# Kernel tuning notes

Measured on AMD Instinct MI355X. Metric: run time of the kernel, lower is better.

Reference implementation:

```python
import jax, jax.numpy as jnp
import numpy as np
import math

# ---- static config (matches init_kwargs) ----
B, L, CIN = 16, 192, 21
D = 128          # d_model
LAYERS = 2
P, S = 24, 12    # patch_length, stride
PRED, COUT = 96, 21
BN_EPS = 1e-5
NT = L // S      # number of patches = 16


def _conv1d(x, w, b=None, stride=1, padding=0):
    # x: (N, Cin, L), w: (Cout, Cin, K)
    y = jax.lax.conv_general_dilated(x, w, (stride,), [(padding, padding)],
                                     dimension_numbers=("NCH", "OIH", "NCH"))
    if b is not None:
        y = y + b[None, :, None]
    return y


def _conv2d(x, w, padding):
    # x: (N, Cin, H, W), w: (Cout, Cin, kh, kw)
    return jax.lax.conv_general_dilated(x, w, (1, 1), padding,
                                        dimension_numbers=("NCHW", "OIHW", "NCHW"))


def _pos_embed(length, d):
    pos = jnp.arange(length, dtype=jnp.float32)[:, None]
    div = jnp.exp(jnp.arange(0, d, 2, dtype=jnp.float32) * (-math.log(10000.0) / d))
    pe = jnp.zeros((length, d), jnp.float32)
    pe = pe.at[:, 0::2].set(jnp.sin(pos * div)).at[:, 1::2].set(jnp.cos(pos * div))
    return pe


def _times_block(x, Wi, pw, pb, g, beta, aw):
    # x: (b, c, t, h, w); Wi: (out=c, in=c, 3, 3)
    b, c, t, h, w = x.shape
    res = x
    pp = x.mean(axis=(3, 4))                       # AdaptiveAvgPool3d((None,1,1)) -> (b,c,t)
    pp = _conv1d(pp, pw, pb, padding=1)            # period_conv
    scale = g / jnp.sqrt(1.0 + BN_EPS)             # eval-mode BN, running stats (0, 1)
    pp = jax.nn.relu(pp * scale[None, :, None] + beta[None, :, None])
    pooled = pp.mean(axis=-1)                      # AdaptiveAvgPool1d(1) -> (b,c)
    alpha = jnp.einsum("oc,bc->bo", aw, pooled) + 1.0   # alpha_conv (1x1, no bias) + 1
    # dynamic weight: (b, out, in, 3, 3) -> (b*out, in, 3, 3)
    Wd = (Wi[None] * alpha[:, :, None, None, None]).reshape(b * c, c, 3, 3)
    x2 = x.reshape(b, c, t, h * w)
    # conv2d with groups=1: every sample sees ALL b*out filters -> (b, b*out, t-2, hw-2)
    y = _conv2d(x2, Wd, [(0, 0), (0, 0)])
    # conv_transpose2d(y, Wd) == conv2d(y, flip(Wd).swap(O,I), full padding)
    Wt = jnp.swapaxes(jnp.flip(Wd, (-2, -1)), 0, 1)     # (c, b*out, 3, 3)
    z = _conv2d(y, Wt, [(2, 2), (2, 2)])                 # (b, c, t, hw)
    return z.reshape(b, c, t, h, w) + res


def setup_inputs() -> dict:
    key = jax.random.key(0)
    ks = jax.random.split(key, 13)
    rn = lambda k, shp, s: jax.random.normal(k, shp, jnp.float32) * s
    return {
        "x": jax.random.normal(ks[0], (B, L, CIN), jnp.float32),
        "token_w": rn(ks[1], (D, CIN, 3), 1.0 / np.sqrt(CIN * 3)),
        "patch_w": rn(ks[2], (P, 1, P), 1.0 / np.sqrt(P)),
        "patch_b": rn(ks[3], (P,), 0.02),
        "Wi": rn(ks[4], (LAYERS, D, D, 3, 3), 1.0 / np.sqrt(D * 9)),
        "pconv_w": rn(ks[5], (LAYERS, D, D, 3), 1.0 / np.sqrt(D * 3)),
        "pconv_b": rn(ks[6], (LAYERS, D), 0.02),
        "bn_g": jnp.ones((LAYERS, D), jnp.float32),
        "bn_b": jnp.zeros((LAYERS, D), jnp.float32),
        "aconv_w": rn(ks[7], (LAYERS, D, D), 1.0 / np.sqrt(D)),
        "fc1_w": rn(ks[8], (PRED, 2 * L), 1.0 / np.sqrt(2 * L)),
        "fc1_b": rn(ks[9], (PRED,), 0.02),
        "fc2_w": rn(ks[10], (COUT, D), 1.0 / np.sqrt(D)),
        "fc2_b": rn(ks[11], (COUT,), 0.02),
    }


def reference(x, token_w, patch_w, patch_b, Wi, pconv_w, pconv_b,
              bn_g, bn_b, aconv_w, fc1_w, fc1_b, fc2_w, fc2_b):
    # ---- DataEmbedding (dropout in eval mode) ----
    xt = jnp.pad(x.transpose(0, 2, 1), ((0, 0), (0, 0), (1, 1)), mode="wrap")  # circular pad
    emb = _conv1d(xt, token_w).transpose(0, 2, 1)            # (B, L, D)
    emb = emb + _pos_embed(L, D)[None]
    # ---- patch Embedding ----
    xe = emb.reshape(B * D, 1, L)                             # matches torch reshape/permute
    xe = jnp.pad(xe, ((0, 0), (0, 0), (0, P - S)), mode="edge")  # replicate pad
    xe = _conv1d(xe, patch_w, patch_b, stride=S)              # (B*D, P, NT)
    xe = xe.transpose(0, 2, 1).reshape(B, NT, P, D)           # torch reshape semantics (C-order)
    x5 = jnp.stack([xe[:, :, 0::2, :], xe[:, :, 1::2, :]], axis=2)  # (B, NT, 2, P//2, D)
    x5 = x5.transpose(0, 4, 1, 2, 3)                          # (B, D, NT, 2, 12)
    # ---- TimesBlocks ----
    for i in range(LAYERS):
        x5 = _times_block(x5, Wi[i], pconv_w[i], pconv_b[i], bn_g[i], bn_b[i], aconv_w[i])
    # ---- heads ----
    xf = x5.reshape(B, -1, D)                                 # (B, 2L, D)
    y1 = xf.transpose(0, 2, 1) @ fc1_w.T + fc1_b              # (B, D, PRED)
    out = y1.transpose(0, 2, 1) @ fc2_w.T + fc2_b             # (B, PRED, COUT)
    return out
```

## Files before the change

### kernel.cpp

```cpp
#include <hip/hip_runtime.h>
#include <math.h>

constexpr int cB = 16, cL = 192, cCIN = 21, cD = 128;
constexpr int cNT = 16, cHW = 24;
constexpr int cPRED = 96, cCOUT = 21;
constexpr int cYH = 14, cYW = 22;

typedef __attribute__((ext_vector_type(8))) short bf16x8;
typedef __attribute__((ext_vector_type(4))) float f32x4;

__device__ inline unsigned short f2bf(float f) {
    union { float f; unsigned u; } v; v.f = f;
    unsigned u = v.u;
    unsigned r = (u + 0x7fffu + ((u >> 16) & 1u)) >> 16;
    return (unsigned short)r;
}

__device__ inline f32x4 mfma16(bf16x8 a, bf16x8 b, f32x4 c) {
    return __builtin_amdgcn_mfma_f32_16x16x32_bf16(a, b, c, 0, 0, 0);
}

__global__ void k_init(const float* __restrict__ Wi, const float* __restrict__ fc1_w,
                       const float* __restrict__ token_w, const float* __restrict__ fc2_w,
                       unsigned short* __restrict__ Wp, unsigned short* __restrict__ w1p,
                       float* __restrict__ twT, unsigned short* __restrict__ w2p,
                       float* __restrict__ w2s, float* __restrict__ peT,
                       unsigned short* __restrict__ Y0T) {
    int e = blockIdx.x * blockDim.x + threadIdx.x;
    if (e < 589824) {
        int lyr = e / 294912;
        int rem = e % 294912;
        int dir = rem / 147456;
        int q = rem % 147456;
        int kt = q >> 12;
        int oi = (q >> 9) & 7;
        int kg = (q >> 7) & 3;
        int r  = (q >> 3) & 15;
        int j  = q & 7;
        int k = kt * 32 + kg * 8 + j;
        int a = k >> 7;
        int o, c;
        if (dir == 0) { o = oi * 16 + r; c = k & 127; }
        else          { o = k & 127;     c = oi * 16 + r; }
        Wp[e] = f2bf(Wi[lyr * 147456 + o * 1152 + c * 9 + a]);
        return;
    }
    e -= 589824;
    if (e < 36864) {
        int p = e / 384, mh = e % 384;
        w1p[e] = f2bf(fc1_w[p * 384 + 3 * (mh & 127) + (mh >> 7)]);
        return;
    }
    e -= 36864;
    if (e < 8064) {
        int d = e & 127, c3 = e >> 7;
        twT[e] = token_w[d * 63 + c3];
        return;
    }
    e -= 8064;
    if (e < 4096) {
        int q = e >> 7, d = e & 127;
        w2p[e] = (q < 21) ? f2bf(fc2_w[q * 128 + d]) : (unsigned short)0;
        return;
    }
    e -= 4096;
    if (e < 32) {
        if (e < 21) {
            float s = 0.f;
            for (int d = 0; d < 128; ++d) s += fc2_w[e * 128 + d];
            w2s[e] = s;
        } else if (e < 32) w2s[e] = 0.f;
        return;
    }
    e -= 32;
    if (e < 24576) {
        int l = e >> 7, d = e & 127;
        int i2 = d >> 1;
        float dv = expf(-(float)(2 * i2) * (9.210340371976184f / 128.f));
        float ang = (float)l * dv;
        peT[e] = (d & 1) ? cosf(ang) : sinf(ang);
        return;
    }
    e -= 24576;
    if (e < 16384) {
        int n = e >> 10, j = e & 1023;
        bf16x8 z = {0, 0, 0, 0, 0, 0, 0, 0};
        *(bf16x8*)(Y0T + n * 65536 + j * 8) = z;
    }
}

__global__ void k_embed(const float* __restrict__ x, const float* __restrict__ twT,
                        const float* __restrict__ peT, float* __restrict__ emb) {
    int idx = blockIdx.x * blockDim.x + threadIdx.x;
    if (idx >= cB * cL * cD) return;
    int d = idx & 127;
    int r = idx >> 7;
    int l = r % cL;
    int b = r / cL;
    int lm = (l == 0) ? 191 : l - 1;
    int lp = (l == 191) ? 0 : l + 1;
    const float* xb = x + b * 4032;
    float acc = peT[l * 128 + d];
    for (int c = 0; c < cCIN; ++c) {
        float x0 = xb[lm * 21 + c], x1 = xb[l * 21 + c], x2 = xb[lp * 21 + c];
        const float* tb = twT + c * 384 + d;
        acc += x0 * tb[0] + x1 * tb[128] + x2 * tb[256];
    }
    emb[idx] = acc;
}

__global__ __launch_bounds__(192) void k_patch(const float* __restrict__ emb,
                                               const float* __restrict__ pw,
                                               const float* __restrict__ pb,
                                               float* __restrict__ x5) {
    __shared__ float pwL[24][24];
    int t = threadIdx.x;
    for (int z = t; z < 576; z += 192) pwL[z / 24][z % 24] = pw[z];
    __syncthreads();
    int pair = blockIdx.x * 8 + t / 24;
    int p = t % 24;
    int i = pair >> 4, tt = pair & 15;
    const float* ebase = emb + i * 192;
    int j0 = tt * 12;
    float acc = pb[p];
    #pragma unroll
    for (int k = 0; k < 24; ++k) {
        int j = j0 + k;
        j = j > 191 ? 191 : j;
        acc += ebase[j] * pwL[p][k];
    }
    int G = (i & 127) * 384 + tt * 24 + p;
    int b = i >> 7;
    int tp = G / 3072;
    int pp2 = (G % 3072) / 128;
    int cc = G & 127;
    x5[b * 49152 + cc * 384 + tp * 24 + (pp2 & 1) * 12 + (pp2 >> 1)] = acc;
}

__global__ __launch_bounds__(256) void k_stats(const float* __restrict__ x5,
        const float* __restrict__ pw, const float* __restrict__ pb,
        const float* __restrict__ g, const float* __restrict__ bb,
        const float* __restrict__ aw, float* __restrict__ alpha,
        unsigned short* __restrict__ XT, int pack) {
    __shared__ float ppT[18][128];
    __shared__ float part[256];
    __shared__ float pooled[128];
    __shared__ unsigned short tile[64][136];
    int b = blockIdx.x, t = threadIdx.x;
    if (t < 128) { ppT[0][t] = 0.f; ppT[17][t] = 0.f; }
    #pragma unroll
    for (int i = 0; i < 8; ++i) {
        int ct = t + 256 * i;
        const float* p = x5 + b * 49152 + ct * 24;
        float s = 0.f;
        #pragma unroll
        for (int j = 0; j < 6; ++j) {
            f32x4 v = *(const f32x4*)(p + 4 * j);
            s += v[0] + v[1] + v[2] + v[3];
        }
        ppT[1 + (ct & 15)][ct >> 4] = s * (1.f / 24.f);
    }
    __syncthreads();
    int o = t >> 1, th = (t & 1) * 8;
    float acc[8];
    float pbo = pb[o];
    #pragma unroll
    for (int i = 0; i < 8; ++i) acc[i] = pbo;
    for (int c4 = 0; c4 < 32; ++c4) {
        union { f32x4 v[3]; float f[12]; } u;
        u.v[0] = *(const f32x4*)(pw + o * 384 + c4 * 12);
        u.v[1] = *(const f32x4*)(pw + o * 384 + c4 * 12 + 4);
        u.v[2] = *(const f32x4*)(pw + o * 384 + c4 * 12 + 8);
        f32x4 pv[10];
        #pragma unroll
        for (int r = 0; r < 10; ++r) pv[r] = *(f32x4*)&ppT[th + r][c4 * 4];
        #pragma unroll
        for (int cc = 0; cc < 4; ++cc) {
            float a0 = u.f[cc * 3], a1 = u.f[cc * 3 + 1], a2 = u.f[cc * 3 + 2];
            #pragma unroll
            for (int i = 0; i < 8; ++i)
                acc[i] += a0 * pv[i][cc] + a1 * pv[i + 1][cc] + a2 * pv[i + 2][cc];
        }
    }
    float scale = g[o] * rsqrtf(1.f + 1e-5f);
    float beta = bb[o];
    float partial = 0.f;
    #pragma unroll
    for (int i = 0; i < 8; ++i) {
        float v = acc[i] * scale + beta;
        partial += v > 0.f ? v : 0.f;
    }
    part[t] = partial;
    __syncthreads();
    if (t < 128) pooled[t] = (part[2 * t] + part[2 * t + 1]) * (1.f / 16.f);
    __syncthreads();
    if (t < 128) {
        float a = 1.f;
        for (int c4 = 0; c4 < 32; ++c4) {
            f32x4 av = *(const f32x4*)(aw + t * 128 + c4 * 4);
            f32x4 pv4 = *(f32x4*)&pooled[c4 * 4];
            a += av[0] * pv4[0] + av[1] * pv4[1] + av[2] * pv4[2] + av[3] * pv4[3];
        }
        alpha[b * 128 + t] = a;
    }
    if (!pack) return;
    for (int ch = 0; ch < 6; ++ch) {
        __syncthreads();
        int p4 = (t & 15) * 4;
        #pragma unroll
        for (int i = 0; i < 8; ++i) {
            int c = (t >> 4) + i * 16;
            f32x4 v = *(const f32x4*)(x5 + b * 49152 + c * 384 + ch * 64 + p4);
            #pragma unroll
            for (int r = 0; r < 4; ++r) tile[p4 + r][c] = f2bf(v[r]);
        }
        __syncthreads();
        #pragma unroll
        for (int i = 0; i < 4; ++i) {
            int idx = t + i * 256;
            int pp = idx >> 4, c8 = (idx & 15) * 8;
            *(bf16x8*)(XT + b * 57344 + (ch * 64 + pp) * 128 + c8) = *(bf16x8*)&tile[pp][c8];
        }
    }
    bf16x8 z = {0, 0, 0, 0, 0, 0, 0, 0};
    #pragma unroll
    for (int i = 0; i < 4; ++i) {
        int idx = t + i * 256;
        int pp = idx >> 4, c8 = (idx & 15) * 8;
        *(bf16x8*)(XT + b * 57344 + (384 + pp) * 128 + c8) = z;
    }
}

__global__ __launch_bounds__(64) void k_gfwd(const unsigned short* __restrict__ XT,
        const unsigned short* __restrict__ Wp, const float* __restrict__ alpha,
        unsigned short* __restrict__ Y0T) {
    int bid = blockIdx.x;
    int rm = bid >> 1, cn = bid & 1;
    int n = rm / 12, p0 = (rm % 12) * 32;
    int o0 = cn * 64;
    int l = threadIdx.x;
    int sm = l & 15, skg = l >> 4;
    const unsigned short* XTn = XT + n * 57344;
    const unsigned short* WB = Wp + (o0 >> 4) * 512 + l * 8;
    f32x4 acc[2][4];
    #pragma unroll
    for (int mi = 0; mi < 2; ++mi)
        #pragma unroll
        for (int ni = 0; ni < 4; ++ni) acc[mi][ni] = (f32x4){0.f, 0.f, 0.f, 0.f};
    #pragma unroll
    for (int kt = 0; kt < 36; ++kt) {
        int a = kt >> 2;
        int off = (a / 3) * 24 + (a % 3);
        int kc = (kt & 3) * 32 + skg * 8;
        const unsigned short* ab = XTn + (p0 + sm + off) * 128 + kc;
        bf16x8 a0 = *(const bf16x8*)(ab);
        bf16x8 a1 = *(const bf16x8*)(ab + 2048);
        const unsigned short* wb = WB + kt * 4096;
        bf16x8 b0 = *(const bf16x8*)(wb);
        bf16x8 b1 = *(const bf16x8*)(wb + 512);
        bf16x8 b2 = *(const bf16x8*)(wb + 1024);
        bf16x8 b3 = *(const bf16x8*)(wb + 1536);
        acc[0][0] = mfma16(a0, b0, acc[0][0]);
        acc[0][1] = mfma16(a0, b1, acc[0][1]);
        acc[0][2] = mfma16(a0, b2, acc[0][2]);
        acc[0][3] = mfma16(a0, b3, acc[0][3]);
        acc[1][0] = mfma16(a1, b0, acc[1][0]);
        acc[1][1] = mfma16(a1, b1, acc[1][1]);
        acc[1][2] = mfma16(a1, b2, acc[1][2]);
        acc[1][3] = mfma16(a1, b3, acc[1][3]);
    }
    #pragma unroll
    for (int ni = 0; ni < 4; ++ni) {
        int o = o0 + ni * 16 + sm;
        float s = 0.f;
        #pragma unroll
        for (int bb2 = 0; bb2 < 16; ++bb2) { float a = alpha[bb2 * 128 + o]; s += a * a; }
        #pragma unroll
        for (int mi = 0; mi < 2; ++mi) {
            #pragma unroll
            for (int r = 0; r < 4; ++r) {
                int p = p0 + mi * 16 + skg * 4 + r;
                bool valid = ((p % 24) < cYW) && ((p / 24) < cYH);
                float v = valid ? acc[mi][ni][r] * s : 0.f;
                Y0T[n * 65536 + (64 + p) * 128 + o] = f2bf(v);
            }
        }
    }
}

__global__ __launch_bounds__(64) void k_gbwd(const unsigned short* __restrict__ Y0T,
        const unsigned short* __restrict__ Wpb, float* __restrict__ x5,
        unsigned short* __restrict__ xdst, int mode) {
    __shared__ unsigned short tr[32][72];
    int bid = blockIdx.x;
    int rm = bid >> 1, cn = bid & 1;
    int n = rm / 12, p0 = (rm % 12) * 32;
    int c0 = cn * 64;
    int l = threadIdx.x;
    int sm = l & 15, skg = l >> 4;
    const unsigned short* Yn = Y0T + n * 65536 + 64 * 128;
    const unsigned short* WB = Wpb + (c0 >> 4) * 512 + l * 8;
    f32x4 acc[2][4];
    #pragma unroll
    for (int mi = 0; mi < 2; ++mi)
        #pragma unroll
        for (int ni = 0; ni < 4; ++ni) acc[mi][ni] = (f32x4){0.f, 0.f, 0.f, 0.f};
    #pragma unroll
    for (int kt = 0; kt < 36; ++kt) {
        int a = kt >> 2;
        int off = (a / 3) * 24 + (a % 3);
        int kc = (kt & 3) * 32 + skg * 8;
        const unsigned short* ab = Yn + (p0 + sm - off) * 128 + kc;
        bf16x8 a0 = *(const bf16x8*)(ab);
        bf16x8 a1 = *(const bf16x8*)(ab + 2048);
        const unsigned short* wb = WB + kt * 4096;
        bf16x8 b0 = *(const bf16x8*)(wb);
        bf16x8 b1 = *(const bf16x8*)(wb + 512);
        bf16x8 b2 = *(const bf16x8*)(wb + 1024);
        bf16x8 b3 = *(const bf16x8*)(wb + 1536);
        acc[0][0] = mfma16(a0, b0, acc[0][0]);
        acc[0][1] = mfma16(a0, b1, acc[0][1]);
        acc[0][2] = mfma16(a0, b2, acc[0][2]);
        acc[0][3] = mfma16(a0, b3, acc[0][3]);
        acc[1][0] = mfma16(a1, b0, acc[1][0]);
        acc[1][1] = mfma16(a1, b1, acc[1][1]);
        acc[1][2] = mfma16(a1, b2, acc[1][2]);
        acc[1][3] = mfma16(a1, b3, acc[1][3]);
    }
    #pragma unroll
    for (int ni = 0; ni < 4; ++ni) {
        int cl = ni * 16 + sm;
        int c = c0 + cl;
        #pragma unroll
        for (int mi = 0; mi < 2; ++mi) {
            int pl = mi * 16 + skg * 4;
            float* dst = x5 + n * 49152 + c * 384 + p0 + pl;
            f32x4 ov = *(f32x4*)dst;
            #pragma unroll
            for (int r = 0; r < 4; ++r) {
                ov[r] += acc[mi][ni][r];
                tr[pl + r][cl] = f2bf(ov[r]);
            }
            *(f32x4*)dst = ov;
        }
    }
    __syncthreads();
    if (mode == 0) {
        #pragma unroll
        for (int pass = 0; pass < 4; ++pass) {
            int idx = pass * 64 + l;
            int row = idx >> 3, ch = idx & 7;
            *(bf16x8*)(xdst + n * 57344 + (p0 + row) * 128 + c0 + ch * 8) = *(bf16x8*)&tr[row][ch * 8];
        }
    } else {
        #pragma unroll
        for (int pass = 0; pass < 4; ++pass) {
            int idx = pass * 64 + l;
            int cl = idx >> 2, pl0 = (idx & 3) * 8;
            __attribute__((aligned(16))) unsigned short tmp[8];
            #pragma unroll
            for (int j2 = 0; j2 < 8; ++j2) tmp[j2] = tr[pl0 + j2][cl];
            *(bf16x8*)(xdst + n * 49152 + ((p0 >> 7) * 128 + c0 + cl) * 128 + (p0 & 127) + pl0) =
                *(bf16x8*)tmp;
        }
    }
}

__global__ __launch_bounds__(64) void k_gemmZ(const unsigned short* __restrict__ xfM,
        const unsigned short* __restrict__ w2p, unsigned short* __restrict__ Zt) {
    int bid = blockIdx.x;
    int b = bid / 12, m0 = (bid % 12) * 32;
    int l = threadIdx.x, sm = l & 15, skg = l >> 4;
    f32x4 acc[2][2];
    #pragma unroll
    for (int mi = 0; mi < 2; ++mi)
        #pragma unroll
        for (int ni = 0; ni < 2; ++ni) acc[mi][ni] = (f32x4){0.f, 0.f, 0.f, 0.f};
    #pragma unroll
    for (int kt = 0; kt < 4; ++kt) {
        int kc = kt * 32 + skg * 8;
        const unsigned short* ab = xfM + b * 49152 + (m0 + sm) * 128 + kc;
        bf16x8 a0 = *(const bf16x8*)(ab);
        bf16x8 a1 = *(const bf16x8*)(ab + 2048);
        bf16x8 b0 = *(const bf16x8*)(w2p + sm * 128 + kc);
        bf16x8 b1 = *(const bf16x8*)(w2p + (16 + sm) * 128 + kc);
        acc[0][0] = mfma16(a0, b0, acc[0][0]);
        acc[0][1] = mfma16(a0, b1, acc[0][1]);
        acc[1][0] = mfma16(a1, b0, acc[1][0]);
        acc[1][1] = mfma16(a1, b1, acc[1][1]);
    }
    #pragma unroll
    for (int mi = 0; mi < 2; ++mi)
        #pragma unroll
        for (int ni = 0; ni < 2; ++ni) {
            int q = ni * 16 + sm;
            int mh = m0 + mi * 16 + skg * 4;
            #pragma unroll
            for (int r = 0; r < 4; ++r)
                Zt[b * 12288 + q * 384 + mh + r] = f2bf(acc[mi][ni][r]);
        }
}

__global__ __launch_bounds__(64) void k_gemmO(const unsigned short* __restrict__ w1p,
        const unsigned short* __restrict__ Zt, const float* __restrict__ b1,
        const float* __restrict__ w2s, const float* __restrict__ b2,
        float* __restrict__ out) {
    int bid = blockIdx.x;
    int b = bid / 3, p0 = (bid % 3) * 32;
    int l = threadIdx.x, sm = l & 15, skg = l >> 4;
    f32x4 acc[2][2];
    #pragma unroll
    for (int mi = 0; mi < 2; ++mi)
        #pragma unroll
        for (int ni = 0; ni < 2; ++ni) acc[mi][ni] = (f32x4){0.f, 0.f, 0.f, 0.f};
    #pragma unroll
    for (int kt = 0; kt < 12; ++kt) {
        int kc = kt * 32 + skg * 8;
        const unsigned short* ab = w1p + (p0 + sm) * 384 + kc;
        bf16x8 a0 = *(const bf16x8*)(ab);
        bf16x8 a1 = *(const bf16x8*)(ab + 16 * 384);
        const unsigned short* zb = Zt + b * 12288 + sm * 384 + kc;
        bf16x8 b0 = *(const bf16x8*)(zb);
        bf16x8 b1v = *(const bf16x8*)(zb + 16 * 384);
        acc[0][0] = mfma16(a0, b0, acc[0][0]);
        acc[0][1] = mfma16(a0, b1v, acc[0][1]);
        acc[1][0] = mfma16(a1, b0, acc[1][0]);
        acc[1][1] = mfma16(a1, b1v, acc[1][1]);
    }
    #pragma unroll
    for (int ni = 0; ni < 2; ++ni) {
        int q = ni * 16 + sm;
        if (q < 21) {
            float wsq = w2s[q], bq = b2[q];
            #pragma unroll
            for (int mi = 0; mi < 2; ++mi) {
                #pragma unroll
                for (int r = 0; r < 4; ++r) {
                    int p = p0 + mi * 16 + skg * 4 + r;
                    out[b * 2016 + p * 21 + q] = acc[mi][ni][r] + b1[p] * wsq + bq;
                }
            }
        }
    }
}

extern "C" void kernel_launch(void* const* d_in, const int* in_sizes, int n_in,
                              void* d_out, int out_size, void* d_ws, size_t ws_size,
                              hipStream_t stream) {
    const float* x       = (const float*)d_in[0];
    const float* token_w = (const float*)d_in[1];
    const float* patch_w = (const float*)d_in[2];
    const float* patch_b = (const float*)d_in[3];
    const float* Wi      = (const float*)d_in[4];
    const float* pconv_w = (const float*)d_in[5];
    const float* pconv_b = (const float*)d_in[6];
    const float* bn_g    = (const float*)d_in[7];
    const float* bn_b    = (const float*)d_in[8];
    const float* aconv_w = (const float*)d_in[9];
    const float* fc1_w   = (const float*)d_in[10];
    const float* fc1_b   = (const float*)d_in[11];
    const float* fc2_w   = (const float*)d_in[12];
    const float* fc2_b   = (const float*)d_in[13];
    float* out = (float*)d_out;

    float* ws    = (float*)d_ws;
    float* x5    = ws;
    float* alpha = ws + 786432;
    unsigned short* Wp  = (unsigned short*)(ws + 788480);
    unsigned short* w1p = (unsigned short*)(ws + 1083392);
    unsigned short* w2p = (unsigned short*)(ws + 1101824);
    float* w2s   = ws + 1103872;
    float* twT   = ws + 1103904;
    float* peT   = ws + 1111968;
    float* emb   = ws + 1136544;
    unsigned short* XT  = (unsigned short*)(ws + 1136544 + 393216);
    unsigned short* xfM = XT;
    unsigned short* Y0T = (unsigned short*)(ws + 1136544 + 393216 + 458752);
    unsigned short* Zt  = Y0T;

    k_init<<<2656, 256, 0, stream>>>(Wi, fc1_w, token_w, fc2_w, Wp, w1p, twT, w2p, w2s, peT, Y0T);
    k_embed<<<1536, 256, 0, stream>>>(x, twT, peT, emb);
    k_patch<<<4096, 192, 0, stream>>>(emb, patch_w, patch_b, x5);
    k_stats<<<16, 256, 0, stream>>>(x5, pconv_w, pconv_b, bn_g, bn_b, aconv_w, alpha, XT, 1);
    k_gfwd<<<384, 64, 0, stream>>>(XT, Wp, alpha, Y0T);
    k_gbwd<<<384, 64, 0, stream>>>(Y0T, Wp + 147456, x5, XT, 0);
    k_stats<<<16, 256, 0, stream>>>(x5, pconv_w + 49152, pconv_b + 128, bn_g + 128,
                                    bn_b + 128, aconv_w + 16384, alpha, XT, 0);
    k_gfwd<<<384, 64, 0, stream>>>(XT, Wp + 2 * 147456, alpha, Y0T);
    k_gbwd<<<384, 64, 0, stream>>>(Y0T, Wp + 3 * 147456, x5, xfM, 1);
    k_gemmZ<<<192, 64, 0, stream>>>(xfM, w2p, Zt);
    k_gemmO<<<48, 64, 0, stream>>>(w1p, Zt, fc1_b, w2s, fc2_b, out);
}
```

Measured before the change: 230.1 us.

## Fuse all stages into one persistent kernel with atomic grid barriers

Replaces the eleven separate kernel launches with a single persistent kernel of 256 blocks. The stages are separated by software grid barriers built on global atomics, and each former kernel body becomes a device function indexed by wave. It also folds the positional encoding into the embed step, stages the token weights in shared memory, and writes the bf16 transposed XT directly from the patch step instead of packing it in the stats kernel. This removes launch gaps and intermediate passes, at the cost of spin-wait barriers and idle blocks during the small phases (stats uses only 16 blocks).

```diff
diff --git a/kernel.cpp b/kernel.cpp
--- a/kernel.cpp
+++ b/kernel.cpp
@@ -1,10 +1,10 @@
 #include <hip/hip_runtime.h>
 #include <math.h>
 
-constexpr int cB = 16, cL = 192, cCIN = 21, cD = 128;
-constexpr int cNT = 16, cHW = 24;
-constexpr int cPRED = 96, cCOUT = 21;
+constexpr int cCIN = 21;
 constexpr int cYH = 14, cYW = 22;
+constexpr int NB = 256;
+constexpr int BT = 256;
 
 typedef __attribute__((ext_vector_type(8))) short bf16x8;
 typedef __attribute__((ext_vector_type(4))) float f32x4;
@@ -20,145 +20,47 @@
     return __builtin_amdgcn_mfma_f32_16x16x32_bf16(a, b, c, 0, 0, 0);
 }
 
-__global__ void k_init(const float* __restrict__ Wi, const float* __restrict__ fc1_w,
-                       const float* __restrict__ token_w, const float* __restrict__ fc2_w,
-                       unsigned short* __restrict__ Wp, unsigned short* __restrict__ w1p,
-                       float* __restrict__ twT, unsigned short* __restrict__ w2p,
-                       float* __restrict__ w2s, float* __restrict__ peT,
-                       unsigned short* __restrict__ Y0T) {
-    int e = blockIdx.x * blockDim.x + threadIdx.x;
-    if (e < 589824) {
-        int lyr = e / 294912;
-        int rem = e % 294912;
-        int dir = rem / 147456;
-        int q = rem % 147456;
-        int kt = q >> 12;
-        int oi = (q >> 9) & 7;
-        int kg = (q >> 7) & 3;
-        int r  = (q >> 3) & 15;
-        int j  = q & 7;
-        int k = kt * 32 + kg * 8 + j;
-        int a = k >> 7;
-        int o, c;
-        if (dir == 0) { o = oi * 16 + r; c = k & 127; }
-        else          { o = k & 127;     c = oi * 16 + r; }
-        Wp[e] = f2bf(Wi[lyr * 147456 + o * 1152 + c * 9 + a]);
-        return;
-    }
-    e -= 589824;
-    if (e < 36864) {
-        int p = e / 384, mh = e % 384;
-        w1p[e] = f2bf(fc1_w[p * 384 + 3 * (mh & 127) + (mh >> 7)]);
-        return;
-    }
-    e -= 36864;
-    if (e < 8064) {
-        int d = e & 127, c3 = e >> 7;
-        twT[e] = token_w[d * 63 + c3];
-        return;
-    }
-    e -= 8064;
-    if (e < 4096) {
-        int q = e >> 7, d = e & 127;
-        w2p[e] = (q < 21) ? f2bf(fc2_w[q * 128 + d]) : (unsigned short)0;
-        return;
-    }
-    e -= 4096;
-    if (e < 32) {
-        if (e < 21) {
-            float s = 0.f;
-            for (int d = 0; d < 128; ++d) s += fc2_w[e * 128 + d];
-            w2s[e] = s;
-        } else if (e < 32) w2s[e] = 0.f;
-        return;
-    }
-    e -= 32;
-    if (e < 24576) {
-        int l = e >> 7, d = e & 127;
-        int i2 = d >> 1;
-        float dv = expf(-(float)(2 * i2) * (9.210340371976184f / 128.f));
-        float ang = (float)l * dv;
-        peT[e] = (d & 1) ? cosf(ang) : sinf(ang);
-        return;
-    }
-    e -= 24576;
-    if (e < 16384) {
-        int n = e >> 10, j = e & 1023;
-        bf16x8 z = {0, 0, 0, 0, 0, 0, 0, 0};
-        *(bf16x8*)(Y0T + n * 65536 + j * 8) = z;
-    }
-}
-
-__global__ void k_embed(const float* __restrict__ x, const float* __restrict__ twT,
-                        const float* __restrict__ peT, float* __restrict__ emb) {
-    int idx = blockIdx.x * blockDim.x + threadIdx.x;
-    if (idx >= cB * cL * cD) return;
-    int d = idx & 127;
-    int r = idx >> 7;
-    int l = r % cL;
-    int b = r / cL;
-    int lm = (l == 0) ? 191 : l - 1;
-    int lp = (l == 191) ? 0 : l + 1;
-    const float* xb = x + b * 4032;
-    float acc = peT[l * 128 + d];
-    for (int c = 0; c < cCIN; ++c) {
-        float x0 = xb[lm * 21 + c], x1 = xb[l * 21 + c], x2 = xb[lp * 21 + c];
-        const float* tb = twT + c * 384 + d;
-        acc += x0 * tb[0] + x1 * tb[128] + x2 * tb[256];
-    }
-    emb[idx] = acc;
-}
-
-__global__ __launch_bounds__(192) void k_patch(const float* __restrict__ emb,
-                                               const float* __restrict__ pw,
-                                               const float* __restrict__ pb,
-                                               float* __restrict__ x5) {
-    __shared__ float pwL[24][24];
-    int t = threadIdx.x;
-    for (int z = t; z < 576; z += 192) pwL[z / 24][z % 24] = pw[z];
-    __syncthreads();
-    int pair = blockIdx.x * 8 + t / 24;
-    int p = t % 24;
-    int i = pair >> 4, tt = pair & 15;
-    const float* ebase = emb + i * 192;
-    int j0 = tt * 12;
-    float acc = pb[p];
-    #pragma unroll
-    for (int k = 0; k < 24; ++k) {
-        int j = j0 + k;
-        j = j > 191 ? 191 : j;
-        acc += ebase[j] * pwL[p][k];
-    }
-    int G = (i & 127) * 384 + tt * 24 + p;
-    int b = i >> 7;
-    int tp = G / 3072;
-    int pp2 = (G % 3072) / 128;
-    int cc = G & 127;
-    x5[b * 49152 + cc * 384 + tp * 24 + (pp2 & 1) * 12 + (pp2 >> 1)] = acc;
-}
-
-__global__ __launch_bounds__(256) void k_stats(const float* __restrict__ x5,
+struct SMem {
+    union {
+        float twL[8064];
+        float pwL[576];
+        struct { float ppT[18][128]; float part[256]; float pooled[128]; } st;
+        unsigned short tr[4][32][72];
+    };
+};
+
+__device__ inline void gbar(int* bar, int phase) {
+    __syncthreads();
+    if (threadIdx.x == 0) {
+        __threadfence();
+        __hip_atomic_fetch_add(&bar[phase], 1, __ATOMIC_RELEASE, __HIP_MEMORY_SCOPE_AGENT);
+        while (__hip_atomic_load(&bar[phase], __ATOMIC_ACQUIRE, __HIP_MEMORY_SCOPE_AGENT) < NB) {
+            __builtin_amdgcn_s_sleep(1);
+        }
+    }
+    __syncthreads();
+}
+
+__global__ void k_zbar(int* bar) {
+    if (threadIdx.x < 16) bar[threadIdx.x] = 0;
+}
+
+__device__ void stats_body(int b, int t, const float* __restrict__ x5,
         const float* __restrict__ pw, const float* __restrict__ pb,
         const float* __restrict__ g, const float* __restrict__ bb,
-        const float* __restrict__ aw, float* __restrict__ alpha,
-        unsigned short* __restrict__ XT, int pack) {
-    __shared__ float ppT[18][128];
-    __shared__ float part[256];
-    __shared__ float pooled[128];
-    __shared__ unsigned short tile[64][136];
-    int b = blockIdx.x, t = threadIdx.x;
-    if (t < 128) { ppT[0][t] = 0.f; ppT[17][t] = 0.f; }
+        const float* __restrict__ aw, float* __restrict__ alpha, SMem* s) {
+    if (t < 128) { s->st.ppT[0][t] = 0.f; s->st.ppT[17][t] = 0.f; }
     #pragma unroll
     for (int i = 0; i < 8; ++i) {
         int ct = t + 256 * i;
         const float* p = x5 + b * 49152 + ct * 24;
-        float s = 0.f;
+        float ssum = 0.f;
         #pragma unroll
         for (int j = 0; j < 6; ++j) {
             f32x4 v = *(const f32x4*)(p + 4 * j);
-            s += v[0] + v[1] + v[2] + v[3];
-        }
-        ppT[1 + (ct & 15)][ct >> 4] = s * (1.f / 24.f);
+            ssum += v[0] + v[1] + v[2] + v[3];
+        }
+        s->st.ppT[1 + (ct & 15)][ct >> 4] = ssum * (1.f / 24.f);
     }
     __syncthreads();
     int o = t >> 1, th = (t & 1) * 8;
@@ -173,7 +75,7 @@
         u.v[2] = *(const f32x4*)(pw + o * 384 + c4 * 12 + 8);
         f32x4 pv[10];
         #pragma unroll
-        for (int r = 0; r < 10; ++r) pv[r] = *(f32x4*)&ppT[th + r][c4 * 4];
+        for (int r = 0; r < 10; ++r) pv[r] = *(f32x4*)&s->st.ppT[th + r][c4 * 4];
         #pragma unroll
         for (int cc = 0; cc < 4; ++cc) {
             float a0 = u.f[cc * 3], a1 = u.f[cc * 3 + 1], a2 = u.f[cc * 3 + 2];
@@ -190,55 +92,27 @@
         float v = acc[i] * scale + beta;
         partial += v > 0.f ? v : 0.f;
     }
-    part[t] = partial;
-    __syncthreads();
-    if (t < 128) pooled[t] = (part[2 * t] + part[2 * t + 1]) * (1.f / 16.f);
+    s->st.part[t] = partial;
+    __syncthreads();
+    if (t < 128) s->st.pooled[t] = (s->st.part[2 * t] + s->st.part[2 * t + 1]) * (1.f / 16.f);
     __syncthreads();
     if (t < 128) {
         float a = 1.f;
         for (int c4 = 0; c4 < 32; ++c4) {
             f32x4 av = *(const f32x4*)(aw + t * 128 + c4 * 4);
-            f32x4 pv4 = *(f32x4*)&pooled[c4 * 4];
+            f32x4 pv4 = *(f32x4*)&s->st.pooled[c4 * 4];
             a += av[0] * pv4[0] + av[1] * pv4[1] + av[2] * pv4[2] + av[3] * pv4[3];
         }
         alpha[b * 128 + t] = a;
     }
-    if (!pack) return;
-    for (int ch = 0; ch < 6; ++ch) {
-        __syncthreads();
-        int p4 = (t & 15) * 4;
-        #pragma unroll
-        for (int i = 0; i < 8; ++i) {
-            int c = (t >> 4) + i * 16;
-            f32x4 v = *(const f32x4*)(x5 + b * 49152 + c * 384 + ch * 64 + p4);
-            #pragma unroll
-            for (int r = 0; r < 4; ++r) tile[p4 + r][c] = f2bf(v[r]);
-        }
-        __syncthreads();
-        #pragma unroll
-        for (int i = 0; i < 4; ++i) {
-            int idx = t + i * 256;
-            int pp = idx >> 4, c8 = (idx & 15) * 8;
-            *(bf16x8*)(XT + b * 57344 + (ch * 64 + pp) * 128 + c8) = *(bf16x8*)&tile[pp][c8];
-        }
-    }
-    bf16x8 z = {0, 0, 0, 0, 0, 0, 0, 0};
-    #pragma unroll
-    for (int i = 0; i < 4; ++i) {
-        int idx = t + i * 256;
-        int pp = idx >> 4, c8 = (idx & 15) * 8;
-        *(bf16x8*)(XT + b * 57344 + (384 + pp) * 128 + c8) = z;
-    }
-}
-
-__global__ __launch_bounds__(64) void k_gfwd(const unsigned short* __restrict__ XT,
+}
+
+__device__ void gfwd_body(int wv, int l, const unsigned short* __restrict__ XT,
         const unsigned short* __restrict__ Wp, const float* __restrict__ alpha,
         unsigned short* __restrict__ Y0T) {
-    int bid = blockIdx.x;
-    int rm = bid >> 1, cn = bid & 1;
+    int rm = wv >> 1, cn = wv & 1;
     int n = rm / 12, p0 = (rm % 12) * 32;
     int o0 = cn * 64;
-    int l = threadIdx.x;
     int sm = l & 15, skg = l >> 4;
     const unsigned short* XTn = XT + n * 57344;
     const unsigned short* WB = Wp + (o0 >> 4) * 512 + l * 8;
@@ -288,15 +162,13 @@
     }
 }
 
-__global__ __launch_bounds__(64) void k_gbwd(const unsigned short* __restrict__ Y0T,
+__device__ void gbwd_body(int wv, int l, int wslot, const unsigned short* __restrict__ Y0T,
         const unsigned short* __restrict__ Wpb, float* __restrict__ x5,
-        unsigned short* __restrict__ xdst, int mode) {
-    __shared__ unsigned short tr[32][72];
-    int bid = blockIdx.x;
-    int rm = bid >> 1, cn = bid & 1;
+        unsigned short* __restrict__ xdst, int mode, SMem* s) {
+    unsigned short (*tr)[72] = s->tr[wslot];
+    int rm = wv >> 1, cn = wv & 1;
     int n = rm / 12, p0 = (rm % 12) * 32;
     int c0 = cn * 64;
-    int l = threadIdx.x;
     int sm = l & 15, skg = l >> 4;
     const unsigned short* Yn = Y0T + n * 65536 + 64 * 128;
     const unsigned short* WB = Wpb + (c0 >> 4) * 512 + l * 8;
@@ -344,7 +216,6 @@
             *(f32x4*)dst = ov;
         }
     }
-    __syncthreads();
     if (mode == 0) {
         #pragma unroll
         for (int pass = 0; pass < 4; ++pass) {
@@ -366,11 +237,10 @@
     }
 }
 
-__global__ __launch_bounds__(64) void k_gemmZ(const unsigned short* __restrict__ xfM,
+__device__ void gemmZ_body(int wv, int l, const unsigned short* __restrict__ xfM,
         const unsigned short* __restrict__ w2p, unsigned short* __restrict__ Zt) {
-    int bid = blockIdx.x;
-    int b = bid / 12, m0 = (bid % 12) * 32;
-    int l = threadIdx.x, sm = l & 15, skg = l >> 4;
+    int b = wv / 12, m0 = (wv % 12) * 32;
+    int sm = l & 15, skg = l >> 4;
     f32x4 acc[2][2];
     #pragma unroll
     for (int mi = 0; mi < 2; ++mi)
@@ -401,13 +271,12 @@
         }
 }
 
-__global__ __launch_bounds__(64) void k_gemmO(const unsigned short* __restrict__ w1p,
+__device__ void gemmO_body(int wv, int l, const unsigned short* __restrict__ w1p,
         const unsigned short* __restrict__ Zt, const float* __restrict__ b1,
         const float* __restrict__ w2s, const float* __restrict__ b2,
         float* __restrict__ out) {
-    int bid = blockIdx.x;
-    int b = bid / 3, p0 = (bid % 3) * 32;
-    int l = threadIdx.x, sm = l & 15, skg = l >> 4;
+    int b = wv / 3, p0 = (wv % 3) * 32;
+    int sm = l & 15, skg = l >> 4;
     f32x4 acc[2][2];
     #pragma unroll
     for (int mi = 0; mi < 2; ++mi)
@@ -442,6 +311,158 @@
             }
         }
     }
+}
+
+__global__ __launch_bounds__(BT) void k_all(
+        const float* __restrict__ x, const float* __restrict__ token_w,
+        const float* __restrict__ patch_w, const float* __restrict__ patch_b,
+        const float* __restrict__ Wi, const float* __restrict__ pconv_w,
+        const float* __restrict__ pconv_b, const float* __restrict__ bn_g,
+        const float* __restrict__ bn_b, const float* __restrict__ aconv_w,
+        const float* __restrict__ fc1_w, const float* __restrict__ fc1_b,
+        const float* __restrict__ fc2_w, const float* __restrict__ fc2_b,
+        float* __restrict__ out,
+        float* __restrict__ x5, float* __restrict__ alpha,
+        unsigned short* __restrict__ Wp, unsigned short* __restrict__ w1p,
+        unsigned short* __restrict__ w2p, float* __restrict__ w2s,
+        float* __restrict__ emb, unsigned short* __restrict__ XT,
+        unsigned short* __restrict__ Y0T, int* bar) {
+    __shared__ SMem s;
+    int t = threadIdx.x;
+    int g = blockIdx.x * BT + t;
+    int wv = g >> 6;
+    int l = t & 63;
+
+    for (int z = t; z < 8064; z += BT) {
+        int d = z / 63, c3 = z % 63;
+        s.twL[c3 * 128 + d] = token_w[z];
+    }
+    __syncthreads();
+
+    for (int e0 = g; e0 < 1040416; e0 += NB * BT) {
+        int e = e0;
+        if (e < 589824) {
+            int lyr = e / 294912;
+            int rem = e % 294912;
+            int dir = rem / 147456;
+            int q = rem % 147456;
+            int kt = q >> 12;
+            int oi = (q >> 9) & 7;
+            int kg = (q >> 7) & 3;
+            int r  = (q >> 3) & 15;
+            int j  = q & 7;
+            int k = kt * 32 + kg * 8 + j;
+            int a = k >> 7;
+            int o, c;
+            if (dir == 0) { o = oi * 16 + r; c = k & 127; }
+            else          { o = k & 127;     c = oi * 16 + r; }
+            Wp[e] = f2bf(Wi[lyr * 147456 + o * 1152 + c * 9 + a]);
+            continue;
+        }
+        e -= 589824;
+        if (e < 36864) {
+            int p = e / 384, mh = e % 384;
+            w1p[e] = f2bf(fc1_w[p * 384 + 3 * (mh & 127) + (mh >> 7)]);
+            continue;
+        }
+        e -= 36864;
+        if (e < 4096) {
+            int q = e >> 7, d = e & 127;
+            w2p[e] = (q < 21) ? f2bf(fc2_w[q * 128 + d]) : (unsigned short)0;
+            continue;
+        }
+        e -= 4096;
+        if (e < 32) {
+            if (e < 21) {
+                float ssum = 0.f;
+                for (int d = 0; d < 128; ++d) ssum += fc2_w[e * 128 + d];
+                w2s[e] = ssum;
+            } else w2s[e] = 0.f;
+            continue;
+        }
+        e -= 32;
+        if (e < 393216) {
+            int d = e & 127;
+            int r = e >> 7;
+            int ll = r % 192;
+            int b = r / 192;
+            int lm = (ll == 0) ? 191 : ll - 1;
+            int lp = (ll == 191) ? 0 : ll + 1;
+            const float* xb = x + b * 4032;
+            int i2 = d >> 1;
+            float dv = expf(-(float)(2 * i2) * (9.210340371976184f / 128.f));
+            float ang = (float)ll * dv;
+            float acc = (d & 1) ? cosf(ang) : sinf(ang);
+            for (int c = 0; c < cCIN; ++c) {
+                float x0 = xb[lm * 21 + c], x1 = xb[ll * 21 + c], x2 = xb[lp * 21 + c];
+                acc += x0 * s.twL[(c * 3 + 0) * 128 + d]
+                     + x1 * s.twL[(c * 3 + 1) * 128 + d]
+                     + x2 * s.twL[(c * 3 + 2) * 128 + d];
+            }
+            emb[e] = acc;
+            continue;
+        }
+        e -= 393216;
+        {
+            int n = e >> 10, j = e & 1023;
+            bf16x8 z = {0, 0, 0, 0, 0, 0, 0, 0};
+            *(bf16x8*)(Y0T + n * 65536 + j * 8) = z;
+        }
+    }
+    gbar(bar, 0);
+
+    for (int z = t; z < 576; z += BT) ((float*)s.pwL)[z] = patch_w[z];
+    __syncthreads();
+    for (int u = g; u < 786432; u += NB * BT) {
+        int pair = u / 24;
+        int p = u % 24;
+        int i = pair >> 4, tt = pair & 15;
+        const float* ebase = emb + i * 192;
+        int j0 = tt * 12;
+        float acc = patch_b[p];
+        #pragma unroll
+        for (int k = 0; k < 24; ++k) {
+            int j = j0 + k;
+            j = j > 191 ? 191 : j;
+            acc += ebase[j] * s.pwL[p * 24 + k];
+        }
+        int G = (i & 127) * 384 + tt * 24 + p;
+        int b = i >> 7;
+        int tp = G / 3072;
+        int pp2 = (G % 3072) / 128;
+        int cc = G & 127;
+        int pp = tp * 24 + (pp2 & 1) * 12 + (pp2 >> 1);
+        x5[b * 49152 + cc * 384 + pp] = acc;
+        XT[b * 57344 + pp * 128 + cc] = f2bf(acc);
+    }
+    if (g < 16384) {
+        int n = g >> 10, rem = g & 1023;
+        int pp = 384 + (rem >> 4), c8 = (rem & 15) * 8;
+        bf16x8 z = {0, 0, 0, 0, 0, 0, 0, 0};
+        *(bf16x8*)(XT + n * 57344 + pp * 128 + c8) = z;
+    }
+    gbar(bar, 1);
+
+    if (blockIdx.x < 16)
+        stats_body(blockIdx.x, t, x5, pconv_w, pconv_b, bn_g, bn_b, aconv_w, alpha, &s);
+    gbar(bar, 2);
+    if (wv < 384) gfwd_body(wv, l, XT, Wp, alpha, Y0T);
+    gbar(bar, 3);
+    if (wv < 384) gbwd_body(wv, l, t >> 6, Y0T, Wp + 147456, x5, XT, 0, &s);
+    gbar(bar, 4);
+
+    if (blockIdx.x < 16)
+        stats_body(blockIdx.x, t, x5, pconv_w + 49152, pconv_b + 128, bn_g + 128,
+                   bn_b + 128, aconv_w + 16384, alpha, &s);
+    gbar(bar, 5);
+    if (wv < 384) gfwd_body(wv, l, XT, Wp + 294912, alpha, Y0T);
+    gbar(bar, 6);
+    if (wv < 384) gbwd_body(wv, l, t >> 6, Y0T, Wp + 442368, x5, XT , 1, &s);
+    gbar(bar, 7);
+
+    if (wv < 192) gemmZ_body(wv, l, XT , w2p, Y0T );
+    gbar(bar, 8);
+    if (wv < 48) gemmO_body(wv, l, w1p, Y0T , fc1_b, w2s, fc2_b, out);
 }
 
 extern "C" void kernel_launch(void* const* d_in, const int* in_sizes, int n_in,
@@ -470,24 +491,13 @@
     unsigned short* w1p = (unsigned short*)(ws + 1083392);
     unsigned short* w2p = (unsigned short*)(ws + 1101824);
     float* w2s   = ws + 1103872;
-    float* twT   = ws + 1103904;
-    float* peT   = ws + 1111968;
     float* emb   = ws + 1136544;
-    unsigned short* XT  = (unsigned short*)(ws + 1136544 + 393216);
-    unsigned short* xfM = XT;
-    unsigned short* Y0T = (unsigned short*)(ws + 1136544 + 393216 + 458752);
-    unsigned short* Zt  = Y0T;
-
-    k_init<<<2656, 256, 0, stream>>>(Wi, fc1_w, token_w, fc2_w, Wp, w1p, twT, w2p, w2s, peT, Y0T);
-    k_embed<<<1536, 256, 0, stream>>>(x, twT, peT, emb);
-    k_patch<<<4096, 192, 0, stream>>>(emb, patch_w, patch_b, x5);
-    k_stats<<<16, 256, 0, stream>>>(x5, pconv_w, pconv_b, bn_g, bn_b, aconv_w, alpha, XT, 1);
-    k_gfwd<<<384, 64, 0, stream>>>(XT, Wp, alpha, Y0T);
-    k_gbwd<<<384, 64, 0, stream>>>(Y0T, Wp + 147456, x5, XT, 0);
-    k_stats<<<16, 256, 0, stream>>>(x5, pconv_w + 49152, pconv_b + 128, bn_g + 128,
-                                    bn_b + 128, aconv_w + 16384, alpha, XT, 0);
-    k_gfwd<<<384, 64, 0, stream>>>(XT, Wp + 2 * 147456, alpha, Y0T);
-    k_gbwd<<<384, 64, 0, stream>>>(Y0T, Wp + 3 * 147456, x5, xfM, 1);
-    k_gemmZ<<<192, 64, 0, stream>>>(xfM, w2p, Zt);
-    k_gemmO<<<48, 64, 0, stream>>>(w1p, Zt, fc1_b, w2s, fc2_b, out);
-}
+    unsigned short* XT  = (unsigned short*)(ws + 1529760);
+    unsigned short* Y0T = (unsigned short*)(ws + 1988512);
+    int* bar     = (int*)(ws + 2514944);
+
+    k_zbar<<<1, 64, 0, stream>>>(bar);
+    k_all<<<NB, BT, 0, stream>>>(x, token_w, patch_w, patch_b, Wi, pconv_w, pconv_b,
+                                 bn_g, bn_b, aconv_w, fc1_w, fc1_b, fc2_w, fc2_b,
+                                 out, x5, alpha, Wp, w1p, w2p, w2s, emb, XT, Y0T, bar);
+}
```

Measured after the change: 733.3 us. 219% more time.
